# Kernel optimization log

Measured on AMD Instinct MI355X. Metric: run time of the kernel, lower is better.

## Reference

```python
import jax, jax.numpy as jnp
import numpy as np

B, S, H = 8, 2048, 1024

def setup_inputs() -> dict:
    key = jax.random.key(0)
    ks = jax.random.split(key, 7)
    scale = 1.0 / np.sqrt(H)
    return {
        "x": jax.random.normal(ks[0], (B, S, H), dtype=jnp.float32),
        "Wq": jax.random.uniform(ks[1], (H, H), jnp.float32, -scale, scale),
        "bq": jax.random.uniform(ks[2], (H,), jnp.float32, -scale, scale),
        "Wk": jax.random.uniform(ks[3], (H, H), jnp.float32, -scale, scale),
        "bk": jax.random.uniform(ks[4], (H,), jnp.float32, -scale, scale),
        "Wv": jax.random.uniform(ks[5], (H, H), jnp.float32, -scale, scale),
        "bv": jax.random.uniform(ks[6], (H,), jnp.float32, -scale, scale),
    }

def reference(x, Wq, bq, Wk, bk, Wv, bv):
    # nn.Linear: x @ W.T + b  (dropout_rate=0.0 -> identity)
    q = jnp.einsum("bsh,oh->bso", x, Wq) + bq
    k = jnp.einsum("bsh,oh->bso", x, Wk) + bk
    v = jnp.einsum("bsh,oh->bso", x, Wv) + bv
    # NOTE: original module applies NO 1/sqrt(d) scaling
    scores = jnp.einsum("bqh,bkh->bqk", q, k)  # [B,S,S]
    probs = jax.nn.softmax(scores, axis=-1)
    context = jnp.einsum("bqk,bkh->bqh", probs, v)  # [B,S,H]
    return context
```

## Files before the change

### kernel.cpp

```cpp
#include <hip/hip_runtime.h>
#include <stdint.h>

typedef unsigned short UST;
typedef __attribute__((ext_vector_type(8))) short    bf16x8;
typedef __attribute__((ext_vector_type(4))) float    f32x4;
typedef __attribute__((ext_vector_type(4))) float    float4_t;
typedef __attribute__((ext_vector_type(4))) UST      ushort4_t;
typedef __attribute__((ext_vector_type(8))) UST      ushort8_t;

__device__ __forceinline__ UST f2bf(float f) {
    union { float f; uint32_t u; } c; c.f = f;
    uint32_t u = c.u;
    u = (u + 0x7FFFu + ((u >> 16) & 1u)) >> 16;
    return (UST)u;
}
__device__ __forceinline__ float bf2f(UST h) {
    union { uint32_t u; float f; } c; c.u = ((uint32_t)h) << 16;
    return c.f;
}

__device__ __forceinline__ void async_copy16(const void* g, void* l) {
    __builtin_amdgcn_global_load_lds(
        (const __attribute__((address_space(1))) uint32_t*)g,
        (__attribute__((address_space(3))) uint32_t*)l, 16, 0, 0);
}

__device__ __forceinline__ void xcd_remap(int& bx, int& by, int& bz) {
    const int gx = (int)gridDim.x, gy = (int)gridDim.y, gz = (int)gridDim.z;
    const int nwg = gx * gy * gz;
    if (nwg & 7) return;
    int flat = ((int)blockIdx.z * gy + (int)blockIdx.y) * gx + (int)blockIdx.x;
    const int q = nwg >> 3;
    int s = (flat & 7) * q + (flat >> 3);
    bx = s % gx; s /= gx;
    by = s % gy;
    bz = s / gy;
}

__global__ void split_kernel(const float* __restrict__ in, UST* __restrict__ hi,
                             UST* __restrict__ lo, int n4) {
    int i = blockIdx.x * blockDim.x + threadIdx.x;
    int stride = gridDim.x * blockDim.x;
    for (; i < n4; i += stride) {
        float4_t v = *(const float4_t*)(in + (size_t)i * 4);
        ushort4_t h, l;
#pragma unroll
        for (int j = 0; j < 4; j++) {
            float f = v[j];
            UST hh = f2bf(f);
            h[j] = hh;
            l[j] = f2bf(f - bf2f(hh));
        }
        *(ushort4_t*)(hi + (size_t)i * 4) = h;
        *(ushort4_t*)(lo + (size_t)i * 4) = l;
    }
}

__global__ void cvt_hi_kernel(const float* __restrict__ in, UST* __restrict__ hi, int n4) {
    int i = blockIdx.x * blockDim.x + threadIdx.x;
    int stride = gridDim.x * blockDim.x;
    for (; i < n4; i += stride) {
        float4_t v = *(const float4_t*)(in + (size_t)i * 4);
        ushort4_t h;
#pragma unroll
        for (int j = 0; j < 4; j++) h[j] = f2bf(v[j]);
        *(ushort4_t*)(hi + (size_t)i * 4) = h;
    }
}

template <int OUT_MODE, bool HAS_BIAS>
__global__ __launch_bounds__(512, 2)
void gemm3_256(const UST* __restrict__ Ah, const UST* __restrict__ Al,
               const UST* __restrict__ Bh, const UST* __restrict__ Bl,
               const float* __restrict__ bias,
               void* __restrict__ C0, void* __restrict__ C1,
               int K, int ldc,
               long long sA, long long sB, long long sC) {
    constexpr int TILE = 8192;
    constexpr int HALF = 4 * TILE;
    __shared__ UST lds[2 * HALF];

    int bx = (int)blockIdx.x, by = (int)blockIdx.y, bz = (int)blockIdx.z;
    xcd_remap(bx, by, bz);
    const int brow = by * 256;
    const int bcol = bx * 256;

    const int t = threadIdx.x;
    const int wave = t >> 6, lane = t & 63;
    const int wr = (wave >> 2) * 128;
    const int wc = (wave & 3) * 64;
    const int lr = lane & 15, lg = lane >> 4;

    const int srow0 = t >> 2;
    const int scol_sw = (((t & 3) ^ ((srow0 >> 1) & 3))) * 8;

    int offA[8], offB[4];
#pragma unroll
    for (int m = 0; m < 8; m++) {
        int r = wr + m * 16 + lr;
        offA[m] = r * 32 + ((lg ^ ((r >> 1) & 3)) << 3);
    }
#pragma unroll
    for (int n = 0; n < 4; n++) {
        int r = wc + n * 16 + lr;
        offB[n] = r * 32 + ((lg ^ ((r >> 1) & 3)) << 3);
    }

    f32x4 acc[8][4];
#pragma unroll
    for (int m = 0; m < 8; m++)
#pragma unroll
        for (int n = 0; n < 4; n++) acc[m][n] = (f32x4){0.f, 0.f, 0.f, 0.f};

    const UST* pAh = Ah + (long long)bz * sA;
    const UST* pAl = Al + (long long)bz * sA;
    const UST* pBh = Bh + (long long)bz * sB;
    const UST* pBl = Bl + (long long)bz * sB;

    auto stage = [&](UST* dst, int k0) {
        const UST* gAh = pAh + (size_t)(brow + srow0) * (size_t)K + k0 + scol_sw;
        async_copy16(gAh, dst + t * 8);
        async_copy16(gAh + (size_t)128 * K, dst + 4096 + t * 8);
        const UST* gAl = pAl + (size_t)(brow + srow0) * (size_t)K + k0 + scol_sw;
        async_copy16(gAl, dst + TILE + t * 8);
        async_copy16(gAl + (size_t)128 * K, dst + TILE + 4096 + t * 8);
        const UST* gBh = pBh + (size_t)(bcol + srow0) * (size_t)K + k0 + scol_sw;
        async_copy16(gBh, dst + 2 * TILE + t * 8);
        async_copy16(gBh + (size_t)128 * K, dst + 2 * TILE + 4096 + t * 8);
        const UST* gBl = pBl + (size_t)(bcol + srow0) * (size_t)K + k0 + scol_sw;
        async_copy16(gBl, dst + 3 * TILE + t * 8);
        async_copy16(gBl + (size_t)128 * K, dst + 3 * TILE + 4096 + t * 8);
    };

    stage(lds, 0);
    int cur = 0;
    const int nt = K / 32;
    for (int it = 0; it < nt; ++it) {
        UST* buf = lds + cur * HALF;
        __builtin_amdgcn_s_barrier();
        if (it + 1 < nt) {
            stage(lds + (cur ^ 1) * HALF, (it + 1) * 32);
            asm volatile("s_waitcnt vmcnt(8)" ::: "memory");
        } else {
            asm volatile("s_waitcnt vmcnt(0)" ::: "memory");
        }
        __builtin_amdgcn_sched_barrier(0);
        __builtin_amdgcn_s_barrier();

        bf16x8 a_[8], b_[4];
#pragma unroll
        for (int m = 0; m < 8; m++) a_[m] = *(const bf16x8*)(buf + offA[m]);
#pragma unroll
        for (int n = 0; n < 4; n++) b_[n] = *(const bf16x8*)(buf + 2 * TILE + offB[n]);
        __builtin_amdgcn_s_setprio(1);
#pragma unroll
        for (int m = 0; m < 8; m++)
#pragma unroll
            for (int n = 0; n < 4; n++)
                acc[m][n] = __builtin_amdgcn_mfma_f32_16x16x32_bf16(a_[m], b_[n], acc[m][n], 0, 0, 0);
        __builtin_amdgcn_s_setprio(0);
#pragma unroll
        for (int n = 0; n < 4; n++) b_[n] = *(const bf16x8*)(buf + 3 * TILE + offB[n]);
        __builtin_amdgcn_s_setprio(1);
#pragma unroll
        for (int m = 0; m < 8; m++)
#pragma unroll
            for (int n = 0; n < 4; n++)
                acc[m][n] = __builtin_amdgcn_mfma_f32_16x16x32_bf16(a_[m], b_[n], acc[m][n], 0, 0, 0);
        __builtin_amdgcn_s_setprio(0);
#pragma unroll
        for (int m = 0; m < 8; m++) a_[m] = *(const bf16x8*)(buf + TILE + offA[m]);
#pragma unroll
        for (int n = 0; n < 4; n++) b_[n] = *(const bf16x8*)(buf + 2 * TILE + offB[n]);
        __builtin_amdgcn_s_setprio(1);
#pragma unroll
        for (int m = 0; m < 8; m++)
#pragma unroll
            for (int n = 0; n < 4; n++)
                acc[m][n] = __builtin_amdgcn_mfma_f32_16x16x32_bf16(a_[m], b_[n], acc[m][n], 0, 0, 0);
        __builtin_amdgcn_s_setprio(0);
        cur ^= 1;
    }

    float bvv[4];
#pragma unroll
    for (int n = 0; n < 4; n++)
        bvv[n] = HAS_BIAS ? bias[bcol + wc + n * 16 + lr] : 0.0f;

#pragma unroll
    for (int m = 0; m < 8; m++) {
        const int row0 = brow + wr + m * 16 + lg * 4;
#pragma unroll
        for (int n = 0; n < 4; n++) {
            const int col = bcol + wc + n * 16 + lr;
            if constexpr (OUT_MODE == 0) {
                float* C = (float*)C0 + (long long)bz * sC;
#pragma unroll
                for (int j = 0; j < 4; j++)
                    C[(size_t)(row0 + j) * ldc + col] = acc[m][n][j] + bvv[n];
            } else {
                UST* Hh = (UST*)C0 + (long long)bz * sC;
                UST* Ll = (UST*)C1 + (long long)bz * sC;
#pragma unroll
                for (int j = 0; j < 4; j++) {
                    float v = acc[m][n][j] + bvv[n];
                    UST h = f2bf(v);
                    Hh[(size_t)(row0 + j) * ldc + col] = h;
                    Ll[(size_t)(row0 + j) * ldc + col] = f2bf(v - bf2f(h));
                }
            }
        }
    }
}

template <int OUT_MODE, bool HAS_BIAS>
__global__ __launch_bounds__(256, 2)
void gemm_bt(const UST* __restrict__ Aptr, const UST* __restrict__ Bptr,
             const float* __restrict__ bias,
             void* __restrict__ C0,
             int K, int ldc,
             long long sA, long long sB, long long sC) {
    constexpr int HALF = 8192;
    __shared__ UST lds[16384];

    int bx = (int)blockIdx.x, by = (int)blockIdx.y, bz = (int)blockIdx.z;
    xcd_remap(bx, by, bz);
    const int brow = by * 128;
    const int bcol = bx * 128;

    const int t = threadIdx.x;
    const int wave = t >> 6, lane = t & 63;
    const int wr = (wave >> 1) * 64, wc = (wave & 1) * 64;
    const int lr = lane & 15, lg = lane >> 4;

    const int srow = t >> 2;
    const int scol_sw = (((t & 3) ^ ((srow >> 1) & 3))) * 8;

    int offA[4], offB[4];
#pragma unroll
    for (int m = 0; m < 4; m++) {
        int r = wr + m * 16 + lr;
        offA[m] = r * 32 + ((lg ^ ((r >> 1) & 3)) << 3);
    }
#pragma unroll
    for (int n = 0; n < 4; n++) {
        int r = wc + n * 16 + lr;
        offB[n] = r * 32 + ((lg ^ ((r >> 1) & 3)) << 3);
    }

    f32x4 acc[4][4];
#pragma unroll
    for (int m = 0; m < 4; m++)
#pragma unroll
        for (int n = 0; n < 4; n++) acc[m][n] = (f32x4){0.f, 0.f, 0.f, 0.f};

    const UST* Ah = Aptr + (long long)bz * sA;
    const UST* Bh = Bptr + (long long)bz * sB;

    auto stage = [&](UST* dst, int k0) {
        const UST* gA = Ah + (size_t)(brow + srow) * (size_t)K + k0 + scol_sw;
        async_copy16(gA, dst + t * 8);
        async_copy16(gA + (size_t)64 * K, dst + 2048 + t * 8);
        const UST* gB = Bh + (size_t)(bcol + srow) * (size_t)K + k0 + scol_sw;
        async_copy16(gB, dst + 4096 + t * 8);
        async_copy16(gB + (size_t)64 * K, dst + 6144 + t * 8);
    };

    stage(lds, 0);
    int cur = 0;
    const int nt = K / 32;
    for (int it = 0; it < nt; ++it) {
        UST* buf = lds + cur * HALF;
        __builtin_amdgcn_s_barrier();
        if (it + 1 < nt) {
            stage(lds + (cur ^ 1) * HALF, (it + 1) * 32);
            asm volatile("s_waitcnt vmcnt(4)" ::: "memory");
        } else {
            asm volatile("s_waitcnt vmcnt(0)" ::: "memory");
        }
        __builtin_amdgcn_sched_barrier(0);
        __builtin_amdgcn_s_barrier();

        bf16x8 ah[4], bh[4];
#pragma unroll
        for (int m = 0; m < 4; m++) ah[m] = *(const bf16x8*)(buf + offA[m]);
#pragma unroll
        for (int n = 0; n < 4; n++) bh[n] = *(const bf16x8*)(buf + 4096 + offB[n]);

        __builtin_amdgcn_s_setprio(1);
#pragma unroll
        for (int m = 0; m < 4; m++)
#pragma unroll
            for (int n = 0; n < 4; n++)
                acc[m][n] = __builtin_amdgcn_mfma_f32_16x16x32_bf16(ah[m], bh[n], acc[m][n], 0, 0, 0);
        __builtin_amdgcn_s_setprio(0);
        cur ^= 1;
    }

    float bvv[4];
#pragma unroll
    for (int n = 0; n < 4; n++)
        bvv[n] = HAS_BIAS ? bias[bcol + wc + n * 16 + lr] : 0.0f;

    if constexpr (OUT_MODE == 2) {
        __syncthreads();
#pragma unroll
        for (int m = 0; m < 4; m++) {
            const int r0 = wr + m * 16 + lg * 4;
#pragma unroll
            for (int n = 0; n < 4; n++) {
                const int c = wc + n * 16 + lr;
                ushort4_t pk;
#pragma unroll
                for (int j = 0; j < 4; j++) pk[j] = f2bf(acc[m][n][j] + bvv[n]);
                *(ushort4_t*)(lds + c * 128 + r0) = pk;
            }
        }
        __syncthreads();
        UST* V = (UST*)C0 + (long long)bz * sC;
        const int hl = t >> 1, soff = (t & 1) * 64;
        const UST* src = lds + hl * 128 + soff;
        UST* dst = V + (size_t)(bcol + hl) * ldc + brow + soff;
#pragma unroll
        for (int i = 0; i < 8; i++)
            *(ushort8_t*)(dst + i * 8) = *(const ushort8_t*)(src + i * 8);
        return;
    }

#pragma unroll
    for (int m = 0; m < 4; m++) {
        const int row0 = brow + wr + m * 16 + lg * 4;
#pragma unroll
        for (int n = 0; n < 4; n++) {
            const int col = bcol + wc + n * 16 + lr;
            float* C = (float*)C0 + (long long)bz * sC;
#pragma unroll
            for (int j = 0; j < 4; j++)
                C[(size_t)(row0 + j) * ldc + col] = acc[m][n][j] + bvv[n];
        }
    }
}

__global__ __launch_bounds__(256)
void softmax_bf16(const float* __restrict__ S, UST* __restrict__ P) {
    const size_t row = blockIdx.x;
    const float* s = S + row * 2048;
    const int t = threadIdx.x;
    const int wave = t >> 6, lane = t & 63;

    float4_t v0 = *(const float4_t*)(s + t * 8);
    float4_t v1 = *(const float4_t*)(s + t * 8 + 4);
    float vv[8];
#pragma unroll
    for (int j = 0; j < 4; j++) { vv[j] = v0[j]; vv[4 + j] = v1[j]; }

    float m = vv[0];
#pragma unroll
    for (int j = 1; j < 8; j++) m = fmaxf(m, vv[j]);
#pragma unroll
    for (int off = 32; off; off >>= 1) m = fmaxf(m, __shfl_xor(m, off));

    __shared__ float red[16];
    if (lane == 0) red[wave] = m;
    __syncthreads();
    m = fmaxf(fmaxf(red[0], red[1]), fmaxf(red[2], red[3]));

    float e[8];
    float sum = 0.f;
#pragma unroll
    for (int j = 0; j < 8; j++) { e[j] = __expf(vv[j] - m); sum += e[j]; }
#pragma unroll
    for (int off = 32; off; off >>= 1) sum += __shfl_xor(sum, off);
    if (lane == 0) red[8 + wave] = sum;
    __syncthreads();
    sum = red[8] + red[9] + red[10] + red[11];

    float inv = 1.0f / sum;
    ushort8_t pk;
#pragma unroll
    for (int j = 0; j < 8; j++) pk[j] = f2bf(e[j] * inv);
    *(ushort8_t*)(P + row * 2048 + t * 8) = pk;
}

extern "C" void kernel_launch(void* const* d_in, const int* in_sizes, int n_in,
                              void* d_out, int out_size, void* d_ws, size_t ws_size,
                              hipStream_t stream) {
    (void)in_sizes; (void)n_in; (void)out_size;
    const float* x  = (const float*)d_in[0];
    const float* Wq = (const float*)d_in[1];
    const float* bq = (const float*)d_in[2];
    const float* Wk = (const float*)d_in[3];
    const float* bk = (const float*)d_in[4];
    const float* Wv = (const float*)d_in[5];
    const float* bv = (const float*)d_in[6];
    float* out = (float*)d_out;

    const int B = 8, S = 2048, H = 1024;
    const size_t BSH = (size_t)B * S * H;
    const long long sXH = (long long)S * H;

    char* p = (char*)d_ws;
    UST* qh = (UST*)p; p += BSH * 2;
    UST* ql = (UST*)p; p += BSH * 2;
    UST* kh = (UST*)p; p += BSH * 2;
    UST* kl = (UST*)p; p += BSH * 2;
    UST* vt = (UST*)p; p += BSH * 2;

    const size_t fixed = (size_t)(p - (char*)d_ws);
    const size_t perB = (size_t)S * S * 6;
    const size_t avail = ws_size > fixed ? ws_size - fixed : 0;

    const size_t HH = (size_t)H * H;

    char* q = p;
    UST* xh  = (UST*)q; q += BSH * 2;
    UST* xl  = (UST*)q; q += BSH * 2;
    UST* wqh = (UST*)q; q += HH * 2;
    UST* wql = (UST*)q; q += HH * 2;
    UST* wkh = (UST*)q; q += HH * 2;
    UST* wkl = (UST*)q; q += HH * 2;
    UST* wvh = (UST*)q; q += HH * 2;

    dim3 blk(256);
    dim3 blk512(512);

    split_kernel<<<2048, blk, 0, stream>>>(x, xh, xl, (int)(BSH / 4));
    split_kernel<<<256, blk, 0, stream>>>(Wq, wqh, wql, (int)(HH / 4));
    split_kernel<<<256, blk, 0, stream>>>(Wk, wkh, wkl, (int)(HH / 4));
    cvt_hi_kernel<<<256, blk, 0, stream>>>(Wv, wvh, (int)(HH / 4));

    dim3 gproj3(H / 256, S / 256, B);
    gemm3_256<1, true><<<gproj3, blk512, 0, stream>>>(
        xh, xl, wqh, wql, bq, qh, ql, H, H, sXH, 0, sXH);
    gemm3_256<1, true><<<gproj3, blk512, 0, stream>>>(
        xh, xl, wkh, wkl, bk, kh, kl, H, H, sXH, 0, sXH);
    dim3 gprojv(H / 128, S / 128, B);
    gemm_bt<2, true><<<gprojv, blk, 0, stream>>>(
        xh, wvh, bv, vt, H, S, sXH, 0, (long long)H * S);

    int g = (int)(avail / perB);
    if (g >= 1) {
        if (g > 8) g = 8;
        while (8 % g) g--;
        float* scores = (float*)p;
        UST* probs = (UST*)(p + (size_t)g * S * S * 4);

        for (int b0 = 0; b0 < B; b0 += g) {
            const size_t ob = (size_t)b0 * S * H;
            dim3 gsc(S / 256, S / 256, g);
            gemm3_256<0, false><<<gsc, blk512, 0, stream>>>(
                qh + ob, ql + ob, kh + ob, kl + ob, nullptr,
                scores, nullptr, H, S, sXH, sXH, (long long)S * S);

            softmax_bf16<<<g * S, blk, 0, stream>>>(scores, probs);

            dim3 gpv(H / 128, S / 128, g);
            gemm_bt<0, false><<<gpv, blk, 0, stream>>>(
                probs, vt + (size_t)b0 * H * S, nullptr,
                out + ob, S, H,
                (long long)S * S, (long long)H * S, sXH);
        }
    } else {
        int rows = (int)(avail / ((size_t)S * 6 * 256)) * 256;
        if (rows < 256) rows = 256;
        if (rows > S) rows = S;
        float* scores = (float*)p;
        UST* probs = (UST*)(p + (size_t)rows * S * 4);

        for (int b = 0; b < B; b++) {
            for (int r0 = 0; r0 < S; r0 += rows) {
                int rc = S - r0 < rows ? S - r0 : rows;
                const size_t ob = (size_t)b * S * H + (size_t)r0 * H;
                dim3 gsc(S / 256, rc / 256, 1);
                gemm3_256<0, false><<<gsc, blk512, 0, stream>>>(
                    qh + ob, ql + ob, kh + (size_t)b * S * H, kl + (size_t)b * S * H,
                    nullptr, scores, nullptr, H, S, 0, 0, 0);

                softmax_bf16<<<rc, blk, 0, stream>>>(scores, probs);

                dim3 gpv(H / 128, rc / 128, 1);
                gemm_bt<0, false><<<gpv, blk, 0, stream>>>(
                    probs, vt + (size_t)b * H * S, nullptr,
                    out + ob, S, H, 0, 0, 0);
            }
        }
    }
}
```

Before: 586.3 us.

## Split split-bf16 GEMM loop into ping-pong phases interleaving loads and MFMAs

Restructures the main K loop of the split-precision (hi/lo bf16) GEMM into six MFMA phases over half-M subtiles. Each phase is separated by barriers, and the LDS fragment reads and next-tile global-to-LDS prefetches are spread across the phases instead of issued all at the start. The aim is to overlap LDS reads and global prefetch with MFMA work and to lower register pressure by holding only half the A fragments at a time. In exchange it adds many workgroup barriers per iteration and waits on vmcnt(0) at the end of each iteration, which could serialize memory and compute.

Result: faster. 556.7 us (-5.0%).

```diff
diff --git a/kernel.cpp b/kernel.cpp
--- a/kernel.cpp
+++ b/kernel.cpp
@@ -117,68 +117,133 @@
     const UST* pBh = Bh + (long long)bz * sB;
     const UST* pBl = Bl + (long long)bz * sB;
 
-    auto stage = [&](UST* dst, int k0) {
-        const UST* gAh = pAh + (size_t)(brow + srow0) * (size_t)K + k0 + scol_sw;
-        async_copy16(gAh, dst + t * 8);
-        async_copy16(gAh + (size_t)128 * K, dst + 4096 + t * 8);
-        const UST* gAl = pAl + (size_t)(brow + srow0) * (size_t)K + k0 + scol_sw;
-        async_copy16(gAl, dst + TILE + t * 8);
-        async_copy16(gAl + (size_t)128 * K, dst + TILE + 4096 + t * 8);
-        const UST* gBh = pBh + (size_t)(bcol + srow0) * (size_t)K + k0 + scol_sw;
-        async_copy16(gBh, dst + 2 * TILE + t * 8);
-        async_copy16(gBh + (size_t)128 * K, dst + 2 * TILE + 4096 + t * 8);
-        const UST* gBl = pBl + (size_t)(bcol + srow0) * (size_t)K + k0 + scol_sw;
-        async_copy16(gBl, dst + 3 * TILE + t * 8);
-        async_copy16(gBl + (size_t)128 * K, dst + 3 * TILE + 4096 + t * 8);
-    };
-
-    stage(lds, 0);
+    {
+        const UST* gAh = pAh + (size_t)(brow + srow0) * (size_t)K + scol_sw;
+        async_copy16(gAh, lds + t * 8);
+        async_copy16(gAh + (size_t)128 * K, lds + 4096 + t * 8);
+        const UST* gAl = pAl + (size_t)(brow + srow0) * (size_t)K + scol_sw;
+        async_copy16(gAl, lds + TILE + t * 8);
+        async_copy16(gAl + (size_t)128 * K, lds + TILE + 4096 + t * 8);
+        const UST* gBh = pBh + (size_t)(bcol + srow0) * (size_t)K + scol_sw;
+        async_copy16(gBh, lds + 2 * TILE + t * 8);
+        async_copy16(gBh + (size_t)128 * K, lds + 2 * TILE + 4096 + t * 8);
+        const UST* gBl = pBl + (size_t)(bcol + srow0) * (size_t)K + scol_sw;
+        async_copy16(gBl, lds + 3 * TILE + t * 8);
+        async_copy16(gBl + (size_t)128 * K, lds + 3 * TILE + 4096 + t * 8);
+        asm volatile("s_waitcnt vmcnt(0)" ::: "memory");
+        __builtin_amdgcn_s_barrier();
+    }
+
     int cur = 0;
     const int nt = K / 32;
     for (int it = 0; it < nt; ++it) {
-        UST* buf = lds + cur * HALF;
-        __builtin_amdgcn_s_barrier();
-        if (it + 1 < nt) {
-            stage(lds + (cur ^ 1) * HALF, (it + 1) * 32);
-            asm volatile("s_waitcnt vmcnt(8)" ::: "memory");
-        } else {
-            asm volatile("s_waitcnt vmcnt(0)" ::: "memory");
-        }
-        __builtin_amdgcn_sched_barrier(0);
-        __builtin_amdgcn_s_barrier();
-
-        bf16x8 a_[8], b_[4];
-#pragma unroll
-        for (int m = 0; m < 8; m++) a_[m] = *(const bf16x8*)(buf + offA[m]);
-#pragma unroll
-        for (int n = 0; n < 4; n++) b_[n] = *(const bf16x8*)(buf + 2 * TILE + offB[n]);
-        __builtin_amdgcn_s_setprio(1);
-#pragma unroll
-        for (int m = 0; m < 8; m++)
-#pragma unroll
-            for (int n = 0; n < 4; n++)
-                acc[m][n] = __builtin_amdgcn_mfma_f32_16x16x32_bf16(a_[m], b_[n], acc[m][n], 0, 0, 0);
-        __builtin_amdgcn_s_setprio(0);
-#pragma unroll
-        for (int n = 0; n < 4; n++) b_[n] = *(const bf16x8*)(buf + 3 * TILE + offB[n]);
-        __builtin_amdgcn_s_setprio(1);
-#pragma unroll
-        for (int m = 0; m < 8; m++)
-#pragma unroll
-            for (int n = 0; n < 4; n++)
-                acc[m][n] = __builtin_amdgcn_mfma_f32_16x16x32_bf16(a_[m], b_[n], acc[m][n], 0, 0, 0);
-        __builtin_amdgcn_s_setprio(0);
-#pragma unroll
-        for (int m = 0; m < 8; m++) a_[m] = *(const bf16x8*)(buf + TILE + offA[m]);
-#pragma unroll
-        for (int n = 0; n < 4; n++) b_[n] = *(const bf16x8*)(buf + 2 * TILE + offB[n]);
-        __builtin_amdgcn_s_setprio(1);
-#pragma unroll
-        for (int m = 0; m < 8; m++)
-#pragma unroll
-            for (int n = 0; n < 4; n++)
-                acc[m][n] = __builtin_amdgcn_mfma_f32_16x16x32_bf16(a_[m], b_[n], acc[m][n], 0, 0, 0);
-        __builtin_amdgcn_s_setprio(0);
+        UST* buf  = lds + cur * HALF;
+        UST* nbuf = lds + (cur ^ 1) * HALF;
+        const bool pf = (it + 1 < nt);
+        const int k1 = (it + 1) * 32;
+
+        bf16x8 ah_[4], al_[4], bh_[4], bl_[4];
+
+#pragma unroll
+        for (int m = 0; m < 4; m++) ah_[m] = *(const bf16x8*)(buf + offA[m]);
+#pragma unroll
+        for (int n = 0; n < 4; n++) bh_[n] = *(const bf16x8*)(buf + 2 * TILE + offB[n]);
+        if (pf) {
+            const UST* gAh = pAh + (size_t)(brow + srow0) * (size_t)K + k1 + scol_sw;
+            async_copy16(gAh, nbuf + t * 8);
+            async_copy16(gAh + (size_t)128 * K, nbuf + 4096 + t * 8);
+            const UST* gAl = pAl + (size_t)(brow + srow0) * (size_t)K + k1 + scol_sw;
+            async_copy16(gAl, nbuf + TILE + t * 8);
+            async_copy16(gAl + (size_t)128 * K, nbuf + TILE + 4096 + t * 8);
+        }
+        __builtin_amdgcn_s_barrier();
+        asm volatile("s_waitcnt lgkmcnt(0)" ::: "memory");
+        __builtin_amdgcn_sched_barrier(0);
+        __builtin_amdgcn_s_setprio(1);
+#pragma unroll
+        for (int m = 0; m < 4; m++)
+#pragma unroll
+            for (int n = 0; n < 4; n++)
+                acc[m][n] = __builtin_amdgcn_mfma_f32_16x16x32_bf16(ah_[m], bh_[n], acc[m][n], 0, 0, 0);
+        __builtin_amdgcn_s_setprio(0);
+        __builtin_amdgcn_s_barrier();
+
+#pragma unroll
+        for (int m = 0; m < 4; m++) al_[m] = *(const bf16x8*)(buf + TILE + offA[m]);
+        if (pf) {
+            const UST* gBh = pBh + (size_t)(bcol + srow0) * (size_t)K + k1 + scol_sw;
+            async_copy16(gBh, nbuf + 2 * TILE + t * 8);
+            async_copy16(gBh + (size_t)128 * K, nbuf + 2 * TILE + 4096 + t * 8);
+            const UST* gBl = pBl + (size_t)(bcol + srow0) * (size_t)K + k1 + scol_sw;
+            async_copy16(gBl, nbuf + 3 * TILE + t * 8);
+            async_copy16(gBl + (size_t)128 * K, nbuf + 3 * TILE + 4096 + t * 8);
+        }
+        __builtin_amdgcn_s_barrier();
+        asm volatile("s_waitcnt lgkmcnt(0)" ::: "memory");
+        __builtin_amdgcn_sched_barrier(0);
+        __builtin_amdgcn_s_setprio(1);
+#pragma unroll
+        for (int m = 0; m < 4; m++)
+#pragma unroll
+            for (int n = 0; n < 4; n++)
+                acc[m][n] = __builtin_amdgcn_mfma_f32_16x16x32_bf16(al_[m], bh_[n], acc[m][n], 0, 0, 0);
+        __builtin_amdgcn_s_setprio(0);
+        __builtin_amdgcn_s_barrier();
+
+#pragma unroll
+        for (int n = 0; n < 4; n++) bl_[n] = *(const bf16x8*)(buf + 3 * TILE + offB[n]);
+        __builtin_amdgcn_s_barrier();
+        asm volatile("s_waitcnt lgkmcnt(0)" ::: "memory");
+        __builtin_amdgcn_sched_barrier(0);
+        __builtin_amdgcn_s_setprio(1);
+#pragma unroll
+        for (int m = 0; m < 4; m++)
+#pragma unroll
+            for (int n = 0; n < 4; n++)
+                acc[m][n] = __builtin_amdgcn_mfma_f32_16x16x32_bf16(ah_[m], bl_[n], acc[m][n], 0, 0, 0);
+        __builtin_amdgcn_s_setprio(0);
+        __builtin_amdgcn_s_barrier();
+
+#pragma unroll
+        for (int m = 0; m < 4; m++) ah_[m] = *(const bf16x8*)(buf + offA[m + 4]);
+        __builtin_amdgcn_s_barrier();
+        asm volatile("s_waitcnt lgkmcnt(0)" ::: "memory");
+        __builtin_amdgcn_sched_barrier(0);
+        __builtin_amdgcn_s_setprio(1);
+#pragma unroll
+        for (int m = 0; m < 4; m++)
+#pragma unroll
+            for (int n = 0; n < 4; n++)
+                acc[m + 4][n] = __builtin_amdgcn_mfma_f32_16x16x32_bf16(ah_[m], bh_[n], acc[m + 4][n], 0, 0, 0);
+        __builtin_amdgcn_s_setprio(0);
+        __builtin_amdgcn_s_barrier();
+
+#pragma unroll
+        for (int m = 0; m < 4; m++) al_[m] = *(const bf16x8*)(buf + TILE + offA[m + 4]);
+        __builtin_amdgcn_s_barrier();
+        asm volatile("s_waitcnt lgkmcnt(0)" ::: "memory");
+        __builtin_amdgcn_sched_barrier(0);
+        __builtin_amdgcn_s_setprio(1);
+#pragma unroll
+        for (int m = 0; m < 4; m++)
+#pragma unroll
+            for (int n = 0; n < 4; n++)
+                acc[m + 4][n] = __builtin_amdgcn_mfma_f32_16x16x32_bf16(al_[m], bh_[n], acc[m + 4][n], 0, 0, 0);
+        __builtin_amdgcn_s_setprio(0);
+        __builtin_amdgcn_s_barrier();
+
+        asm volatile("s_waitcnt vmcnt(0)" ::: "memory");
+        __builtin_amdgcn_sched_barrier(0);
+        __builtin_amdgcn_s_barrier();
+        __builtin_amdgcn_s_setprio(1);
+#pragma unroll
+        for (int m = 0; m < 4; m++)
+#pragma unroll
+            for (int n = 0; n < 4; n++)
+                acc[m + 4][n] = __builtin_amdgcn_mfma_f32_16x16x32_bf16(ah_[m], bl_[n], acc[m + 4][n], 0, 0, 0);
+        __builtin_amdgcn_s_setprio(0);
+        __builtin_amdgcn_s_barrier();
+
         cur ^= 1;
     }
 
```

## Restructure split-bf16 GEMM as concatenated-K segments with four-slot prefetch

Applied to the files above, without the earlier changes.

The three hi/lo product passes are recast as one long K loop over three segments (Ah·Bh, Al·Bh, Ah·Bl). Each K tile now stages only one A tile and one B tile into a four-slot LDS ring, and two tiles are consumed per barrier-separated iteration. This aims for deeper prefetch and simpler stages with fewer barriers per MFMA. In exchange it drops the reuse of the hi fragments across passes, which raises global-load and LDS-read traffic per MFMA. It also waits on all outstanding loads (vmcnt 0) each iteration.

New measurement: 607.4 us. +3.6%, slower.

```diff
diff --git a/kernel.cpp b/kernel.cpp
--- a/kernel.cpp
+++ b/kernel.cpp
@@ -76,9 +76,8 @@
                void* __restrict__ C0, void* __restrict__ C1,
                int K, int ldc,
                long long sA, long long sB, long long sC) {
-    constexpr int TILE = 8192;
-    constexpr int HALF = 4 * TILE;
-    __shared__ UST lds[2 * HALF];
+    constexpr int SLOT = 16384;
+    __shared__ UST lds[4 * SLOT];
 
     int bx = (int)blockIdx.x, by = (int)blockIdx.y, bz = (int)blockIdx.z;
     xcd_remap(bx, by, bz);
@@ -112,74 +111,70 @@
 #pragma unroll
         for (int n = 0; n < 4; n++) acc[m][n] = (f32x4){0.f, 0.f, 0.f, 0.f};
 
-    const UST* pAh = Ah + (long long)bz * sA;
-    const UST* pAl = Al + (long long)bz * sA;
-    const UST* pBh = Bh + (long long)bz * sB;
-    const UST* pBl = Bl + (long long)bz * sB;
-
-    auto stage = [&](UST* dst, int k0) {
-        const UST* gAh = pAh + (size_t)(brow + srow0) * (size_t)K + k0 + scol_sw;
-        async_copy16(gAh, dst + t * 8);
-        async_copy16(gAh + (size_t)128 * K, dst + 4096 + t * 8);
-        const UST* gAl = pAl + (size_t)(brow + srow0) * (size_t)K + k0 + scol_sw;
-        async_copy16(gAl, dst + TILE + t * 8);
-        async_copy16(gAl + (size_t)128 * K, dst + TILE + 4096 + t * 8);
-        const UST* gBh = pBh + (size_t)(bcol + srow0) * (size_t)K + k0 + scol_sw;
-        async_copy16(gBh, dst + 2 * TILE + t * 8);
-        async_copy16(gBh + (size_t)128 * K, dst + 2 * TILE + 4096 + t * 8);
-        const UST* gBl = pBl + (size_t)(bcol + srow0) * (size_t)K + k0 + scol_sw;
-        async_copy16(gBl, dst + 3 * TILE + t * 8);
-        async_copy16(gBl + (size_t)128 * K, dst + 3 * TILE + 4096 + t * 8);
+    const UST* a0 = Ah + (long long)bz * sA;
+    const UST* a1 = Al + (long long)bz * sA;
+    const UST* b0 = Bh + (long long)bz * sB;
+    const UST* b2 = Bl + (long long)bz * sB;
+
+    const int ktPerSeg = K / 32;
+    const int NT = 3 * ktPerSeg;
+
+    auto stageKT = [&](int kt) {
+        int seg = kt >= 2 * ktPerSeg ? 2 : (kt >= ktPerSeg ? 1 : 0);
+        int koff = (kt - seg * ktPerSeg) << 5;
+        const UST* pA = (seg == 1) ? a1 : a0;
+        const UST* pB = (seg == 2) ? b2 : b0;
+        UST* dst = lds + (kt & 3) * SLOT;
+        const UST* gA = pA + (size_t)(brow + srow0) * (size_t)K + koff + scol_sw;
+        async_copy16(gA, dst + t * 8);
+        async_copy16(gA + (size_t)128 * K, dst + 4096 + t * 8);
+        const UST* gB = pB + (size_t)(bcol + srow0) * (size_t)K + koff + scol_sw;
+        async_copy16(gB, dst + 8192 + t * 8);
+        async_copy16(gB + (size_t)128 * K, dst + 8192 + 4096 + t * 8);
     };
 
-    stage(lds, 0);
-    int cur = 0;
-    const int nt = K / 32;
-    for (int it = 0; it < nt; ++it) {
-        UST* buf = lds + cur * HALF;
-        __builtin_amdgcn_s_barrier();
-        if (it + 1 < nt) {
-            stage(lds + (cur ^ 1) * HALF, (it + 1) * 32);
-            asm volatile("s_waitcnt vmcnt(8)" ::: "memory");
-        } else {
-            asm volatile("s_waitcnt vmcnt(0)" ::: "memory");
-        }
+    stageKT(0);
+    stageKT(1);
+
+    for (int j = 0; j < NT / 2; ++j) {
+        const int kt = 2 * j;
+        asm volatile("s_waitcnt vmcnt(0)" ::: "memory");
         __builtin_amdgcn_sched_barrier(0);
         __builtin_amdgcn_s_barrier();
 
-        bf16x8 a_[8], b_[4];
-#pragma unroll
-        for (int m = 0; m < 8; m++) a_[m] = *(const bf16x8*)(buf + offA[m]);
-#pragma unroll
-        for (int n = 0; n < 4; n++) b_[n] = *(const bf16x8*)(buf + 2 * TILE + offB[n]);
-        __builtin_amdgcn_s_setprio(1);
-#pragma unroll
-        for (int m = 0; m < 8; m++)
-#pragma unroll
-            for (int n = 0; n < 4; n++)
-                acc[m][n] = __builtin_amdgcn_mfma_f32_16x16x32_bf16(a_[m], b_[n], acc[m][n], 0, 0, 0);
-        __builtin_amdgcn_s_setprio(0);
-#pragma unroll
-        for (int n = 0; n < 4; n++) b_[n] = *(const bf16x8*)(buf + 3 * TILE + offB[n]);
-        __builtin_amdgcn_s_setprio(1);
-#pragma unroll
-        for (int m = 0; m < 8; m++)
-#pragma unroll
-            for (int n = 0; n < 4; n++)
-                acc[m][n] = __builtin_amdgcn_mfma_f32_16x16x32_bf16(a_[m], b_[n], acc[m][n], 0, 0, 0);
-        __builtin_amdgcn_s_setprio(0);
-#pragma unroll
-        for (int m = 0; m < 8; m++) a_[m] = *(const bf16x8*)(buf + TILE + offA[m]);
-#pragma unroll
-        for (int n = 0; n < 4; n++) b_[n] = *(const bf16x8*)(buf + 2 * TILE + offB[n]);
-        __builtin_amdgcn_s_setprio(1);
-#pragma unroll
-        for (int m = 0; m < 8; m++)
-#pragma unroll
-            for (int n = 0; n < 4; n++)
-                acc[m][n] = __builtin_amdgcn_mfma_f32_16x16x32_bf16(a_[m], b_[n], acc[m][n], 0, 0, 0);
-        __builtin_amdgcn_s_setprio(0);
-        cur ^= 1;
+        if (kt + 2 < NT) stageKT(kt + 2);
+        if (kt + 3 < NT) stageKT(kt + 3);
+
+        {
+            UST* buf = lds + (kt & 3) * SLOT;
+            bf16x8 a_[8], b_[4];
+#pragma unroll
+            for (int m = 0; m < 8; m++) a_[m] = *(const bf16x8*)(buf + offA[m]);
+#pragma unroll
+            for (int n = 0; n < 4; n++) b_[n] = *(const bf16x8*)(buf + 8192 + offB[n]);
+            __builtin_amdgcn_s_setprio(1);
+#pragma unroll
+            for (int m = 0; m < 8; m++)
+#pragma unroll
+                for (int n = 0; n < 4; n++)
+                    acc[m][n] = __builtin_amdgcn_mfma_f32_16x16x32_bf16(a_[m], b_[n], acc[m][n], 0, 0, 0);
+            __builtin_amdgcn_s_setprio(0);
+        }
+        {
+            UST* buf = lds + ((kt + 1) & 3) * SLOT;
+            bf16x8 a_[8], b_[4];
+#pragma unroll
+            for (int m = 0; m < 8; m++) a_[m] = *(const bf16x8*)(buf + offA[m]);
+#pragma unroll
+            for (int n = 0; n < 4; n++) b_[n] = *(const bf16x8*)(buf + 8192 + offB[n]);
+            __builtin_amdgcn_s_setprio(1);
+#pragma unroll
+            for (int m = 0; m < 8; m++)
+#pragma unroll
+                for (int n = 0; n < 4; n++)
+                    acc[m][n] = __builtin_amdgcn_mfma_f32_16x16x32_bf16(a_[m], b_[n], acc[m][n], 0, 0, 0);
+            __builtin_amdgcn_s_setprio(0);
+        }
     }
 
     float bvv[4];
```
